# Kernel optimization log

Hardware: AMD Instinct MI355X
Metric: run time of the kernel (lower is better)

Reference implementation:

```python
import math
import jax, jax.numpy as jnp
import numpy as np

RADIUS = 1.5
NUM_R = 4
NUM_THETA = 8
C_IN = 8
C_OUT = 8
EPS = 1e-9


def _bilinear_sample_zeros(ker, grid):
    """torch.F.grid_sample(mode='bilinear', padding_mode='zeros', align_corners=False)
    ker:  [C, H, W] (shared across batch, torch expands it)
    grid: [B, M, N, 2] with grid[...,0]=x (W axis), grid[...,1]=y (H axis), in [-1,1]
    returns [C, B, M, N]
    """
    C, H, W = ker.shape
    x, y = grid[..., 0], grid[..., 1]
    ix = ((x + 1.0) * W - 1.0) * 0.5   # unnormalize, align_corners=False
    iy = ((y + 1.0) * H - 1.0) * 0.5
    x0 = jnp.floor(ix)
    y0 = jnp.floor(iy)
    wx = ix - x0
    wy = iy - y0

    def corner(xi, yi, w):
        valid = (xi >= 0) & (xi <= W - 1) & (yi >= 0) & (yi <= H - 1)
        xc = jnp.clip(xi, 0, W - 1).astype(jnp.int32)
        yc = jnp.clip(yi, 0, H - 1).astype(jnp.int32)
        v = ker[:, yc, xc]                        # [C, B, M, N]
        return v * (w * valid)[None]

    return (corner(x0, y0, (1 - wx) * (1 - wy))
            + corner(x0 + 1, y0, wx * (1 - wy))
            + corner(x0, y0 + 1, (1 - wx) * wy)
            + corner(x0 + 1, y0 + 1, wx * wy))


def setup_inputs() -> dict:
    key = jax.random.key(0)
    ks = jax.random.split(key, 4)
    B, M, N = 2, 384, 384
    field = jax.random.normal(ks[0], (B, N, 2), dtype=jnp.float32)
    center = jax.random.normal(ks[1], (B, M, 2), dtype=jnp.float32)
    field_feat = jax.random.normal(ks[2], (B, N, C_IN, 2), dtype=jnp.float32)
    field_mask = jnp.ones((B, N, 1), dtype=jnp.float32)
    kernel = jax.random.normal(ks[3], (C_OUT, C_IN, NUM_R, NUM_THETA, 2, 2), dtype=jnp.float32)
    return {"field": field, "center": center, "field_feat": field_feat,
            "field_mask": field_mask, "kernel": kernel}


def reference(field, center, field_feat, field_mask, kernel):
    B, M = center.shape[0], center.shape[1]
    N = field.shape[1]
    # relative positions, scaled to kernel support
    rel = (field[:, None, :, :] - center[:, :, None, :]) / RADIUS   # [B,M,N,2]
    # polar coordinates
    r = jnp.sqrt(rel[..., 0] ** 2 + rel[..., 1] ** 2 + EPS)          # [B,M,N]
    nonzero = ~((rel[..., 0] == 0.0) & (rel[..., 1] == 0.0))
    theta = jnp.where(nonzero, jnp.arctan2(rel[..., 1], rel[..., 0]), 0.0)
    # grid_sample normalized coords: x over radius axis, y over (padded) theta axis
    gx = 2.0 * r - 1.0
    gy = theta * (1.0 / math.pi) * (NUM_THETA / (NUM_THETA + 2.0))
    grid = jnp.stack([gx, gy], axis=-1)                              # [B,M,N,2]
    # kernel [co,ci,r,th,2,2] -> [co,ci,2,2,r,th] -> [C,r,th], circular-pad theta
    ker = kernel.transpose(0, 1, 4, 5, 2, 3).reshape(-1, NUM_R, NUM_THETA)
    ker = jnp.concatenate([ker[..., -1:], ker, ker[..., :1]], axis=-1)  # [C,r,th+2]
    ker = ker.transpose(0, 2, 1)                                     # [C, th+2, r]
    kof = _bilinear_sample_zeros(ker, grid)                          # [C,B,M,N]
    kof = kof.transpose(1, 2, 3, 0).reshape(B, M, N, C_OUT, C_IN, 2, 2)
    # attention: relu((1 - |rel|^2)^3) masked by field_mask
    att = jax.nn.relu((1.0 - jnp.sum(rel ** 2, axis=-1)) ** 3)[..., None]  # [B,M,N,1]
    att = att * field_mask[:, None]                                  # [B,M,N,1]
    psi = jnp.sum(att, axis=2)[..., 0]                               # [B,M]
    psi = jnp.where(psi == 0.0, 1.0, psi)[:, :, None, None]          # [B,M,1,1]
    aff = field_feat[:, None] * att[..., None]                       # [B,M,N,ci,2]
    out = jnp.einsum('bmnoiyx,bmnix->bmoy', kof, aff)                # [B,M,co,2]
    return out / psi
```

## Files before the change

### kernel.cpp

```cpp
#include <hip/hip_runtime.h>
#include <math.h>

#define B_ 2
#define M_ 384
#define N_ 384
#define NTY 10
#define NSLOT 640

__global__ __launch_bounds__(256) void equiconv_kernel(
    const float* __restrict__ field,
    const float* __restrict__ center,
    const float* __restrict__ feat,
    const float* __restrict__ mask,
    const float* __restrict__ kern,
    float* __restrict__ out) {
  __shared__ int    sX0Y0[N_];
  __shared__ float2 sW[N_];
  __shared__ float4 sG4[N_ * 4];
  __shared__ float  sS4[4][NSLOT];
  __shared__ float  sS[NSLOT];
  __shared__ float  sPartial[16][17];
  __shared__ float  sPsi[4];
  __shared__ int    sCnt;

  int t = threadIdx.x;
  int bm = blockIdx.x;
  int b = bm / M_;

  if (t == 0) sCnt = 0;
  if (t < 4) sPsi[t] = 0.f;
  __syncthreads();

  float cx = center[bm * 2 + 0];
  float cy = center[bm * 2 + 1];
  const float invR = 1.0f / 1.5f;
  const float fourpi = 4.0f / 3.14159265358979323846f;
  float psi_acc = 0.f;

  for (int n = t; n < N_; n += 256) {
    int fn = b * N_ + n;
    float rx = (field[fn * 2 + 0] - cx) * invR;
    float ry = (field[fn * 2 + 1] - cy) * invR;
    float r2 = rx * rx + ry * ry;
    float onem = 1.f - r2;
    float att = onem * onem * onem;
    if (att <= 0.f) continue;
    att *= mask[fn];
    if (att == 0.f) continue;

    psi_acc += att;

    float r = sqrtf(r2 + 1e-9f);
    float theta = (rx == 0.f && ry == 0.f) ? 0.f : atan2f(ry, rx);
    float ix = 4.f * r - 0.5f;
    float iy = theta * fourpi + 4.5f;
    float x0f = floorf(ix), y0f = floorf(iy);
    int x0 = (int)x0f, y0 = (int)y0f;

    int a = atomicAdd(&sCnt, 1);
    sX0Y0[a] = (x0 + 1) | (y0 << 8);
    sW[a] = make_float2(ix - x0f, iy - y0f);
    const float4* fp = (const float4*)(feat + fn * 16);
    float4* gp = &sG4[a * 4];
#pragma unroll
    for (int q = 0; q < 4; ++q) {
      float4 v = fp[q];
      v.x *= att; v.y *= att; v.z *= att; v.w *= att;
      gp[q] = v;
    }
  }

#pragma unroll
  for (int off = 32; off > 0; off >>= 1)
    psi_acc += __shfl_xor(psi_acc, off, 64);
  if ((t & 63) == 0) sPsi[t >> 6] = psi_acc;
  __syncthreads();
  int cnt = sCnt;

  int f  = t & 15;
  int xr = (t >> 4) & 3;
  int w  = t >> 6;
  const float* sG = (const float*)sG4;

  float acc[NTY];
#pragma unroll
  for (int k = 0; k < NTY; ++k) acc[k] = 0.f;

  int chunk = (cnt + 3) >> 2;
  int a0 = w * chunk;
  int a1 = min(a0 + chunk, cnt);
  for (int a = a0; a < a1; ++a) {
    int meta = sX0Y0[a];
    float2 wv = sW[a];
    float g = sG[a * 16 + f];
    int x0 = (meta & 255) - 1;
    int y0 = meta >> 8;
    float wx1 = wv.x, wy1 = wv.y;
    float ux = (xr == x0) ? (1.f - wx1) : ((xr == x0 + 1) ? wx1 : 0.f);
    float ug = ux * g;
    float wy0 = 1.f - wy1;
#pragma unroll
    for (int k = 0; k < NTY; ++k) {
      float vy = (k == y0) ? wy0 : ((k == y0 + 1) ? wy1 : 0.f);
      acc[k] = fmaf(ug, vy, acc[k]);
    }
  }
#pragma unroll
  for (int k = 0; k < NTY; ++k)
    sS4[w][(k * 4 + xr) * 16 + f] = acc[k];
  __syncthreads();

  for (int s = t; s < NSLOT; s += 256)
    sS[s] = sS4[0][s] + sS4[1][s] + sS4[2][s] + sS4[3][s];
  __syncthreads();

  int oy = t & 15, grp = t >> 4;
  int o = oy >> 1, y = oy & 1;
  float cacc = 0.f;
  for (int c = grp; c < 40; c += 16) {
    int ty = c >> 2, cxr = c & 3;
    int th = (ty + 7) & 7;
    const float* sp = &sS[c * 16];
#pragma unroll
    for (int ff = 0; ff < 16; ++ff) {
      int i = ff >> 1, x = ff & 1;
      int idx = ((((o * 8 + i) * 4 + cxr) * 8 + th) * 2 + y) * 2 + x;
      cacc = fmaf(kern[idx], sp[ff], cacc);
    }
  }
  sPartial[grp][oy] = cacc;
  __syncthreads();

  if (t < 16) {
    float sum = 0.f;
#pragma unroll
    for (int gg = 0; gg < 16; ++gg) sum += sPartial[gg][t];
    float psi = sPsi[0] + sPsi[1] + sPsi[2] + sPsi[3];
    if (psi == 0.f) psi = 1.f;
    out[bm * 16 + t] = sum / psi;
  }
}

extern "C" void kernel_launch(void* const* d_in, const int* in_sizes, int n_in,
                              void* d_out, int out_size, void* d_ws, size_t ws_size,
                              hipStream_t stream) {
  (void)in_sizes; (void)n_in; (void)out_size; (void)d_ws; (void)ws_size;
  const float* field  = (const float*)d_in[0];
  const float* center = (const float*)d_in[1];
  const float* feat   = (const float*)d_in[2];
  const float* mask   = (const float*)d_in[3];
  const float* kern   = (const float*)d_in[4];
  float* out = (float*)d_out;

  equiconv_kernel<<<dim3(B_ * M_), dim3(256), 0, stream>>>(
      field, center, feat, mask, kern, out);
}
```

Baseline: 84.26 us.

## Precompute padded kernel table, widen blocks to 8 waves, use scalar metadata loads

Adds a small pre-kernel that rearranges the convolution weights into a theta-padded lookup table in workspace, so the final contraction reads contiguous coalesced values instead of computing scattered indices. The main kernel grows to 512 threads with 8 waves, splitting the neighbour accumulation across more waves, and uses readfirstlane to turn per-neighbour metadata into wave-uniform scalars. Shared buffers are unioned to offset the larger per-wave partial arrays. The cost is an extra kernel launch, a longer cross-wave reduction, and possibly lower occupancy from the bigger blocks.

```diff
diff --git a/kernel.cpp b/kernel.cpp
--- a/kernel.cpp
+++ b/kernel.cpp
@@ -6,29 +6,47 @@
 #define N_ 384
 #define NTY 10
 #define NSLOT 640
+#define NW 8
+#define BS 512
 
-__global__ __launch_bounds__(256) void equiconv_kernel(
+__global__ __launch_bounds__(256) void build_table_kernel(
+    const float* __restrict__ kern, float* __restrict__ table) {
+  int cell = blockIdx.x;
+  int t = threadIdx.x;
+  int f = t >> 4, oy = t & 15;
+  int tw = cell >> 2, xr = cell & 3;
+  int th = (tw == 0) ? 7 : ((tw == 9) ? 0 : (tw - 1));
+  int o = oy >> 1, y = oy & 1, i = f >> 1, x = f & 1;
+  int src = ((((o * 8 + i) * 4 + xr) * 8 + th) * 2 + y) * 2 + x;
+  table[cell * 256 + t] = kern[src];
+}
+
+struct F2 { float x, y; };
+
+union SmemU {
+  struct { int meta[N_]; F2 w[N_]; } a;
+  struct { float S[NSLOT]; float partial[16][17]; } c;
+};
+
+__global__ __launch_bounds__(BS) void equiconv_kernel(
     const float* __restrict__ field,
     const float* __restrict__ center,
     const float* __restrict__ feat,
     const float* __restrict__ mask,
-    const float* __restrict__ kern,
+    const float* __restrict__ table,
     float* __restrict__ out) {
-  __shared__ int    sX0Y0[N_];
-  __shared__ float2 sW[N_];
+  __shared__ SmemU u;
   __shared__ float4 sG4[N_ * 4];
-  __shared__ float  sS4[4][NSLOT];
-  __shared__ float  sS[NSLOT];
-  __shared__ float  sPartial[16][17];
-  __shared__ float  sPsi[4];
-  __shared__ int    sCnt;
+  __shared__ float sS4[NW][NSLOT];
+  __shared__ float sPsi[NW];
+  __shared__ int sCnt;
 
   int t = threadIdx.x;
   int bm = blockIdx.x;
   int b = bm / M_;
 
   if (t == 0) sCnt = 0;
-  if (t < 4) sPsi[t] = 0.f;
+  if (t < NW) sPsi[t] = 0.f;
   __syncthreads();
 
   float cx = center[bm * 2 + 0];
@@ -37,7 +55,7 @@
   const float fourpi = 4.0f / 3.14159265358979323846f;
   float psi_acc = 0.f;
 
-  for (int n = t; n < N_; n += 256) {
+  for (int n = t; n < N_; n += BS) {
     int fn = b * N_ + n;
     float rx = (field[fn * 2 + 0] - cx) * invR;
     float ry = (field[fn * 2 + 1] - cy) * invR;
@@ -58,8 +76,9 @@
     int x0 = (int)x0f, y0 = (int)y0f;
 
     int a = atomicAdd(&sCnt, 1);
-    sX0Y0[a] = (x0 + 1) | (y0 << 8);
-    sW[a] = make_float2(ix - x0f, iy - y0f);
+    u.a.meta[a] = (x0 + 1) | (y0 << 8);
+    u.a.w[a].x = ix - x0f;
+    u.a.w[a].y = iy - y0f;
     const float4* fp = (const float4*)(feat + fn * 16);
     float4* gp = &sG4[a * 4];
 #pragma unroll
@@ -77,65 +96,70 @@
   __syncthreads();
   int cnt = sCnt;
 
-  int f  = t & 15;
-  int xr = (t >> 4) & 3;
-  int w  = t >> 6;
+  int f   = t & 15;
+  int xr4 = (t >> 4) & 3;
+  int w   = t >> 6;
   const float* sG = (const float*)sG4;
 
   float acc[NTY];
 #pragma unroll
   for (int k = 0; k < NTY; ++k) acc[k] = 0.f;
 
-  int chunk = (cnt + 3) >> 2;
+  int chunk = (cnt + NW - 1) / NW;
   int a0 = w * chunk;
   int a1 = min(a0 + chunk, cnt);
+#pragma unroll 2
   for (int a = a0; a < a1; ++a) {
-    int meta = sX0Y0[a];
-    float2 wv = sW[a];
+    int meta = __builtin_amdgcn_readfirstlane(u.a.meta[a]);
+    F2 wv = u.a.w[a];
+    float wx1 = __int_as_float(__builtin_amdgcn_readfirstlane(__float_as_int(wv.x)));
+    float wy1 = __int_as_float(__builtin_amdgcn_readfirstlane(__float_as_int(wv.y)));
     float g = sG[a * 16 + f];
     int x0 = (meta & 255) - 1;
     int y0 = meta >> 8;
-    float wx1 = wv.x, wy1 = wv.y;
-    float ux = (xr == x0) ? (1.f - wx1) : ((xr == x0 + 1) ? wx1 : 0.f);
+    float ux = (xr4 == x0) ? (1.f - wx1) : ((xr4 == x0 + 1) ? wx1 : 0.f);
     float ug = ux * g;
     float wy0 = 1.f - wy1;
 #pragma unroll
     for (int k = 0; k < NTY; ++k) {
       float vy = (k == y0) ? wy0 : ((k == y0 + 1) ? wy1 : 0.f);
-      acc[k] = fmaf(ug, vy, acc[k]);
+      acc[k] = fmaf(vy, ug, acc[k]);
     }
   }
 #pragma unroll
   for (int k = 0; k < NTY; ++k)
-    sS4[w][(k * 4 + xr) * 16 + f] = acc[k];
+    sS4[w][(k * 4 + xr4) * 16 + f] = acc[k];
   __syncthreads();
 
-  for (int s = t; s < NSLOT; s += 256)
-    sS[s] = sS4[0][s] + sS4[1][s] + sS4[2][s] + sS4[3][s];
+  for (int s = t; s < NSLOT; s += BS) {
+    float v = 0.f;
+#pragma unroll
+    for (int ww = 0; ww < NW; ++ww) v += sS4[ww][s];
+    u.c.S[s] = v;
+  }
   __syncthreads();
 
-  int oy = t & 15, grp = t >> 4;
-  int o = oy >> 1, y = oy & 1;
-  float cacc = 0.f;
-  for (int c = grp; c < 40; c += 16) {
-    int ty = c >> 2, cxr = c & 3;
-    int th = (ty + 7) & 7;
-    const float* sp = &sS[c * 16];
+  if (t < 256) {
+    int oy = t & 15, grp = t >> 4;
+    float cacc = 0.f;
+    for (int c = grp; c < 40; c += 16) {
+      const float* tp = table + c * 256 + oy;
+      const float* sp = &u.c.S[c * 16];
 #pragma unroll
-    for (int ff = 0; ff < 16; ++ff) {
-      int i = ff >> 1, x = ff & 1;
-      int idx = ((((o * 8 + i) * 4 + cxr) * 8 + th) * 2 + y) * 2 + x;
-      cacc = fmaf(kern[idx], sp[ff], cacc);
+      for (int ff = 0; ff < 16; ++ff)
+        cacc = fmaf(tp[ff * 16], sp[ff], cacc);
     }
+    u.c.partial[grp][oy] = cacc;
   }
-  sPartial[grp][oy] = cacc;
   __syncthreads();
 
   if (t < 16) {
     float sum = 0.f;
 #pragma unroll
-    for (int gg = 0; gg < 16; ++gg) sum += sPartial[gg][t];
-    float psi = sPsi[0] + sPsi[1] + sPsi[2] + sPsi[3];
+    for (int gg = 0; gg < 16; ++gg) sum += u.c.partial[gg][t];
+    float psi = 0.f;
+#pragma unroll
+    for (int ww = 0; ww < NW; ++ww) psi += sPsi[ww];
     if (psi == 0.f) psi = 1.f;
     out[bm * 16 + t] = sum / psi;
   }
@@ -144,14 +168,16 @@
 extern "C" void kernel_launch(void* const* d_in, const int* in_sizes, int n_in,
                               void* d_out, int out_size, void* d_ws, size_t ws_size,
                               hipStream_t stream) {
-  (void)in_sizes; (void)n_in; (void)out_size; (void)d_ws; (void)ws_size;
+  (void)in_sizes; (void)n_in; (void)out_size; (void)ws_size;
   const float* field  = (const float*)d_in[0];
   const float* center = (const float*)d_in[1];
   const float* feat   = (const float*)d_in[2];
   const float* mask   = (const float*)d_in[3];
   const float* kern   = (const float*)d_in[4];
   float* out = (float*)d_out;
+  float* table = (float*)d_ws;
 
-  equiconv_kernel<<<dim3(B_ * M_), dim3(256), 0, stream>>>(
-      field, center, feat, mask, kern, out);
+  build_table_kernel<<<dim3(40), dim3(256), 0, stream>>>(kern, table);
+  equiconv_kernel<<<dim3(B_ * M_), dim3(BS), 0, stream>>>(
+      field, center, feat, mask, table, out);
 }
```

After: 83.11 us. Within noise of the previous version (-1.4%).
